# Optimization experiments

Hardware: AMD Instinct MI355X
Metric: run time of the kernel (lower is better)

The kernel has to match this reference:

```python
import jax, jax.numpy as jnp
import numpy as np

B, KL, XL, DIM, H, PB = 4, 128, 4096, 256, 8, 8
HD = DIM // H
SCALE = HD ** -0.5
N_DIS = 64 + 2


def setup_inputs() -> dict:
    key = jax.random.key(0)
    ks = jax.random.split(key, 10)
    x = jax.random.normal(ks[0], (B, XL, DIM), jnp.float32)
    kernal = jax.random.normal(ks[1], (B, KL, DIM), jnp.float32)
    rd = jax.random.randint(ks[2], (B, KL, XL), 0, N_DIS)
    polar_pos = jax.random.randint(ks[3], (B, KL, XL), 0, PB)
    att_mask = jax.random.uniform(ks[4], (B, H, XL, KL)) < 0.1
    W_qkv = jax.random.normal(ks[5], (DIM, 3 * DIM), jnp.float32) * 0.02
    dis_embed = jax.random.normal(ks[6], (N_DIS, H), jnp.float32) * 0.02
    polar_emb = jax.random.normal(ks[7], (PB, 1), jnp.float32) * 0.02
    W_proj = jax.random.normal(ks[8], (DIM, DIM), jnp.float32) * 0.02
    b_proj = jnp.zeros((DIM,), jnp.float32)
    return dict(x=x, kernal=kernal, rd=rd, polar_pos=polar_pos, att_mask=att_mask,
                W_qkv=W_qkv, dis_embed=dis_embed, polar_emb=polar_emb,
                W_proj=W_proj, b_proj=b_proj)


def _heads(t, h):
    b, n, d = t.shape
    return t.reshape(b, n, h, d // h).transpose(0, 2, 1, 3)  # b h n hd


def reference(x, kernal, rd, polar_pos, att_mask, W_qkv, dis_embed, polar_emb, W_proj, b_proj):
    b, xl, dim = x.shape
    kl = kernal.shape[1]
    h = H
    scale = (dim // h) ** -0.5

    q, k, v = [_heads(t, h) for t in jnp.split(x @ W_qkv, 3, axis=-1)]        # b h xl hd
    k_q, k_k, k_v = [_heads(t, h) for t in jnp.split(kernal @ W_qkv, 3, axis=-1)]  # b h kl hd

    rd_e = dis_embed[rd].transpose(0, 3, 1, 2)  # (b,kl,xl,h) -> (b,h,kl,xl)

    # kernel -> x attention scores
    k_x_attn = jnp.einsum('bhkd,bhxd->bhkx', k_q, k) * scale  # b h kl xl

    # main orientation: one-hot-weighted |attn| reduced over x, argmax over polar bins
    pp = jnp.broadcast_to(polar_pos[:, None], (b, h, kl, xl))  # b h kl xl
    polar_hot = jax.nn.one_hot(pp, PB, dtype=k_x_attn.dtype)   # b h kl xl o
    ori_sum = jnp.einsum('bhkx,bhkxo->bhko', jnp.abs(k_x_attn), polar_hot)
    main_ori = jnp.argmax(ori_sum, axis=-1)                    # b h kl
    new_polar = pp - main_ori[..., None]
    new_polar = jnp.where(new_polar < 0, new_polar + PB, new_polar)
    polar_bias = polar_emb[new_polar, 0]                       # b h kl xl

    mask_k = att_mask.transpose(0, 1, 3, 2)                    # b h kl xl
    k_x_attn = jnp.where(mask_k, jnp.asarray(-1e6, k_x_attn.dtype), k_x_attn)
    attn_k = jax.nn.softmax(k_x_attn + rd_e + polar_bias, axis=-1)
    k_out = jnp.einsum('bhkx,bhxd->bhkd', attn_k, v)
    k_out = k_out.transpose(0, 2, 1, 3).reshape(b, kl, dim) @ W_proj + b_proj

    # x -> kernel attention scores
    x_k_attn = jnp.einsum('bhxd,bhkd->bhxk', q, k_k) * scale   # b h xl kl
    x_k_attn = jnp.where(att_mask, jnp.asarray(-1e9, x_k_attn.dtype), x_k_attn)
    x_k_attn = jax.nn.softmax(x_k_attn + rd_e.transpose(0, 1, 3, 2)
                              + polar_bias.transpose(0, 1, 3, 2), axis=-1)
    x_out = jnp.einsum('bhxk,bhkd->bhxd', x_k_attn, k_v)
    x_out = x_out.transpose(0, 2, 1, 3).reshape(b, xl, dim) @ W_proj + b_proj

    return (x_out, k_out)
```

## Files before the change

### kernel.cpp

```cpp
#include <hip/hip_runtime.h>
#include <hip/hip_bf16.h>

#define B_    4
#define KL_   128
#define XL_   4096
#define DIM_  256
#define H_    8
#define HD_   32
#define PB_   8
#define NDIS_ 66
#define TDIM_ 768
#define SCALE_ 0.17677669529663687f
#define NS_   4
#define XCH_  (XL_ / NS_)
#define NCH2_ 64
#define KC2_  16

typedef float v4f __attribute__((ext_vector_type(4)));
typedef short v8s __attribute__((ext_vector_type(8)));

__device__ __forceinline__ unsigned short f2bf(float f) {
    __hip_bfloat16 h = __float2bfloat16(f);
    return __builtin_bit_cast(unsigned short, h);
}
__device__ __forceinline__ float bf2f(unsigned short u) {
    return __bfloat162float(__builtin_bit_cast(__hip_bfloat16, u));
}
__device__ __forceinline__ void cvt_hilo(float v, unsigned short& hi, unsigned short& lo) {
    hi = f2bf(v);
    lo = f2bf(v - bf2f(hi));
}

__global__ __launch_bounds__(256) void pack_mask(const int* __restrict__ att_mask,
                                                 unsigned int* __restrict__ mbits) {
    size_t wid = (size_t)blockIdx.x * 256 + threadIdx.x;
    const int* src = &att_mask[wid * 32];
    unsigned bits = 0;
#pragma unroll
    for (int i = 0; i < 8; ++i) {
        int4 m4 = *(const int4*)&src[i * 4];
        bits |= (m4.x ? 1u : 0u) << (i * 4 + 0);
        bits |= (m4.y ? 1u : 0u) << (i * 4 + 1);
        bits |= (m4.z ? 1u : 0u) << (i * 4 + 2);
        bits |= (m4.w ? 1u : 0u) << (i * 4 + 3);
    }
    mbits[wid] = bits;
}

__global__ __launch_bounds__(256) void cvt_mat(const float* __restrict__ A,
                                               unsigned short* __restrict__ Ah,
                                               unsigned short* __restrict__ Al,
                                               size_t n4) {
    size_t i = ((size_t)blockIdx.x * 256 + threadIdx.x);
    if (i >= n4) return;
    float4 v = *(const float4*)&A[i * 4];
    ushort4 h, l;
    cvt_hilo(v.x, h.x, l.x);
    cvt_hilo(v.y, h.y, l.y);
    cvt_hilo(v.z, h.z, l.z);
    cvt_hilo(v.w, h.w, l.w);
    *(ushort4*)&Ah[i * 4] = h;
    *(ushort4*)&Al[i * 4] = l;
}

__global__ __launch_bounds__(256) void cvt_wT(const float* __restrict__ W,
                                              unsigned short* __restrict__ Wh,
                                              unsigned short* __restrict__ Wl,
                                              int K, int N) {
    int n = blockIdx.x, k = threadIdx.x;
    float v = W[(size_t)k * N + n];
    unsigned short h, l;
    cvt_hilo(v, h, l);
    Wh[(size_t)n * K + k] = h;
    Wl[(size_t)n * K + k] = l;
}

__global__ __launch_bounds__(256) void cvt_kq(const float* __restrict__ qkv_k,
                                              unsigned short* __restrict__ Kqh_g,
                                              unsigned short* __restrict__ Kql_g,
                                              unsigned short* __restrict__ Kk_bf,
                                              unsigned short* __restrict__ VT_bf) {
    const int bh = blockIdx.x;
    const int b = bh >> 3, h = bh & 7;
    const int tid = threadIdx.x;
    const int k = tid >> 1, dg = (tid & 1) * 16;
    const float* src = &qkv_k[((size_t)(b * KL_ + k)) * TDIM_ + h * HD_ + dg];
    unsigned short hi[16], lo[16];
#pragma unroll
    for (int j4 = 0; j4 < 4; ++j4) {
        float4 v = *(const float4*)&src[j4 * 4];
        cvt_hilo(v.x, hi[j4 * 4 + 0], lo[j4 * 4 + 0]);
        cvt_hilo(v.y, hi[j4 * 4 + 1], lo[j4 * 4 + 1]);
        cvt_hilo(v.z, hi[j4 * 4 + 2], lo[j4 * 4 + 2]);
        cvt_hilo(v.w, hi[j4 * 4 + 3], lo[j4 * 4 + 3]);
    }
    unsigned short* dh = &Kqh_g[((size_t)bh * KL_ + k) * HD_ + dg];
    unsigned short* dl = &Kql_g[((size_t)bh * KL_ + k) * HD_ + dg];
    *(uint4*)&dh[0] = *(uint4*)&hi[0];
    *(uint4*)&dh[8] = *(uint4*)&hi[8];
    *(uint4*)&dl[0] = *(uint4*)&lo[0];
    *(uint4*)&dl[8] = *(uint4*)&lo[8];
    unsigned short kk[16];
#pragma unroll
    for (int j4 = 0; j4 < 4; ++j4) {
        float4 v = *(const float4*)&src[DIM_ + j4 * 4];
        kk[j4 * 4 + 0] = f2bf(v.x);
        kk[j4 * 4 + 1] = f2bf(v.y);
        kk[j4 * 4 + 2] = f2bf(v.z);
        kk[j4 * 4 + 3] = f2bf(v.w);
    }
    unsigned short* dk = &Kk_bf[((size_t)bh * KL_ + k) * HD_ + dg];
    *(uint4*)&dk[0] = *(uint4*)&kk[0];
    *(uint4*)&dk[8] = *(uint4*)&kk[8];
#pragma unroll
    for (int j = 0; j < 16; ++j)
        VT_bf[((size_t)bh * HD_ + dg + j) * KL_ + k] = f2bf(src[2 * DIM_ + j]);
}

__global__ __launch_bounds__(256) void gemm_mfma(const unsigned short* __restrict__ Ah,
                                                 const unsigned short* __restrict__ Al,
                                                 const unsigned short* __restrict__ Bh,
                                                 const unsigned short* __restrict__ Bl,
                                                 float* __restrict__ C,
                                                 const float* __restrict__ bias,
                                                 int M, int N, int K) {
    __shared__ __align__(16) unsigned short Ah_s[128 * 32];
    __shared__ __align__(16) unsigned short Al_s[128 * 32];
    __shared__ __align__(16) unsigned short Bh_s[128 * 32];
    __shared__ __align__(16) unsigned short Bl_s[128 * 32];
    const int tid = threadIdx.x;
    const int w = tid >> 6, lane = tid & 63;
    const int c = lane & 15, q = lane >> 4;
    const int bm = blockIdx.y * 128, bn = blockIdx.x * 128;

    const int lrow = lane >> 2;
    const int lcol = (lane & 3) * 8;

    v4f acc[2][8] = {};
    for (int k0 = 0; k0 < K; k0 += 32) {
        __syncthreads();
#pragma unroll
        for (int i = 0; i < 2; ++i) {
            const int chunk = w * 2 + i;
            const int row = chunk * 16 + lrow;
            const size_t ga = (size_t)(bm + row) * K + k0 + lcol;
            const size_t gb = (size_t)(bn + row) * K + k0 + lcol;
            const int lo = chunk * 512;
            __builtin_amdgcn_global_load_lds(
                (const __attribute__((address_space(1))) unsigned int*)&Ah[ga],
                (__attribute__((address_space(3))) unsigned int*)&Ah_s[lo], 16, 0, 0);
            __builtin_amdgcn_global_load_lds(
                (const __attribute__((address_space(1))) unsigned int*)&Al[ga],
                (__attribute__((address_space(3))) unsigned int*)&Al_s[lo], 16, 0, 0);
            __builtin_amdgcn_global_load_lds(
                (const __attribute__((address_space(1))) unsigned int*)&Bh[gb],
                (__attribute__((address_space(3))) unsigned int*)&Bh_s[lo], 16, 0, 0);
            __builtin_amdgcn_global_load_lds(
                (const __attribute__((address_space(1))) unsigned int*)&Bl[gb],
                (__attribute__((address_space(3))) unsigned int*)&Bl_s[lo], 16, 0, 0);
        }
        asm volatile("s_waitcnt vmcnt(0)" ::: "memory");
        __syncthreads();
        v8s afh[2], afl[2];
#pragma unroll
        for (int mt = 0; mt < 2; ++mt) {
            afh[mt] = *(v8s*)&Ah_s[(w * 32 + mt * 16 + c) * 32 + q * 8];
            afl[mt] = *(v8s*)&Al_s[(w * 32 + mt * 16 + c) * 32 + q * 8];
        }
#pragma unroll
        for (int nt = 0; nt < 8; ++nt) {
            v8s bfh = *(v8s*)&Bh_s[(nt * 16 + c) * 32 + q * 8];
            v8s bfl = *(v8s*)&Bl_s[(nt * 16 + c) * 32 + q * 8];
#pragma unroll
            for (int mt = 0; mt < 2; ++mt) {
                acc[mt][nt] = __builtin_amdgcn_mfma_f32_16x16x32_bf16(afl[mt], bfh, acc[mt][nt], 0, 0, 0);
                acc[mt][nt] = __builtin_amdgcn_mfma_f32_16x16x32_bf16(afh[mt], bfl, acc[mt][nt], 0, 0, 0);
                acc[mt][nt] = __builtin_amdgcn_mfma_f32_16x16x32_bf16(afh[mt], bfh, acc[mt][nt], 0, 0, 0);
            }
        }
    }
#pragma unroll
    for (int mt = 0; mt < 2; ++mt) {
#pragma unroll
        for (int nt = 0; nt < 8; ++nt) {
            int col = bn + nt * 16 + c;
            float bv = bias ? bias[col] : 0.0f;
#pragma unroll
            for (int r = 0; r < 4; ++r) {
                int row = bm + w * 32 + mt * 16 + q * 4 + r;
                C[(size_t)row * N + col] = acc[mt][nt][r] + bv;
            }
        }
    }
}

__global__ __launch_bounds__(256) void gemm64(const float* __restrict__ A,
                                              const float* __restrict__ Bw,
                                              float* __restrict__ C,
                                              const float* __restrict__ bias,
                                              int M, int N, int K) {
    __shared__ __align__(16) float As[16][68];
    __shared__ __align__(16) float Bs[16][64];
    const int tid = threadIdx.x;
    const int tx = tid & 15, ty = tid >> 4;
    const int bn = blockIdx.x * 64, bm = blockIdx.y * 64;
    const int am = tid >> 2, ac = tid & 3;
    float acc[4][4] = {};
    for (int k0 = 0; k0 < K; k0 += 16) {
        float4 a4 = *(const float4*)&A[(size_t)(bm + am) * K + k0 + ac * 4];
        As[ac * 4 + 0][am] = a4.x;
        As[ac * 4 + 1][am] = a4.y;
        As[ac * 4 + 2][am] = a4.z;
        As[ac * 4 + 3][am] = a4.w;
        *(float4*)&Bs[ty][tx * 4] = *(const float4*)&Bw[(size_t)(k0 + ty) * N + bn + tx * 4];
        __syncthreads();
#pragma unroll
        for (int kk = 0; kk < 16; ++kk) {
            float4 av = *(const float4*)&As[kk][ty * 4];
            float4 bv = *(const float4*)&Bs[kk][tx * 4];
            float a[4] = {av.x, av.y, av.z, av.w};
            float b[4] = {bv.x, bv.y, bv.z, bv.w};
#pragma unroll
            for (int i = 0; i < 4; ++i)
#pragma unroll
                for (int j = 0; j < 4; ++j) acc[i][j] += a[i] * b[j];
        }
        __syncthreads();
    }
#pragma unroll
    for (int i = 0; i < 4; ++i) {
        int m = bm + ty * 4 + i;
#pragma unroll
        for (int j = 0; j < 4; ++j) {
            int n = bn + tx * 4 + j;
            float v = acc[i][j];
            if (bias) v += bias[n];
            C[(size_t)m * N + n] = v;
        }
    }
}

__global__ __launch_bounds__(256) void score_bins_mfma4(const float* __restrict__ qkv_x,
                                                        const unsigned short* __restrict__ Kqh_g,
                                                        const unsigned short* __restrict__ Kql_g,
                                                        const int* __restrict__ rd,
                                                        const int* __restrict__ polar_pos,
                                                        const unsigned int* __restrict__ mbits,
                                                        const float* __restrict__ dis_embed,
                                                        __hip_bfloat16* __restrict__ Sg,
                                                        float* __restrict__ binspart) {
    const int b = blockIdx.z, h = blockIdx.y, xc = blockIdx.x;
    const int x0 = xc * 64;
    const int tid = threadIdx.x;
    const int w = tid >> 6, lane = tid & 63;
    const int c15 = lane & 15, q = lane >> 4;
    const size_t bh = (size_t)(b * H_ + h);

    __shared__ unsigned int mskb[64][5];
    __shared__ float de_h[NDIS_];
    __shared__ float binsL[8][4][16][PB_];
    __shared__ __align__(16) unsigned short Ss[2][16][72];

    {
        int xr = tid >> 2, kg = tid & 3;
        mskb[xr][kg] = mbits[(bh * XL_ + x0 + xr) * 4 + kg];
    }
    if (tid < NDIS_) de_h[tid] = dis_embed[tid * H_ + h];
    __syncthreads();

    v8s axh, axl;
    {
        const float* src = &qkv_x[((size_t)b * XL_ + x0 + w * 16 + c15) * TDIM_ + DIM_ + h * HD_ + q * 8];
        float4 v0 = *(const float4*)&src[0];
        float4 v1 = *(const float4*)&src[4];
        float vv[8] = {v0.x, v0.y, v0.z, v0.w, v1.x, v1.y, v1.z, v1.w};
#pragma unroll
        for (int j = 0; j < 8; ++j) {
            unsigned short hi, lo;
            cvt_hilo(vv[j], hi, lo);
            ((short*)&axh)[j] = (short)hi;
            ((short*)&axl)[j] = (short)lo;
        }
    }

    v8s bqh[2], bql[2];
    int4 r4[2], p4[2];
    auto load_nt = [&](int nt, int s) {
        const int k = nt * 16 + c15;
        const size_t kqoff = (bh * KL_ + k) * HD_ + q * 8;
        bqh[s] = *(const v8s*)&Kqh_g[kqoff];
        bql[s] = *(const v8s*)&Kql_g[kqoff];
        const size_t rowoff = ((size_t)(b * KL_ + k)) * XL_ + x0 + w * 16 + q * 4;
        r4[s] = *(const int4*)&rd[rowoff];
        p4[s] = *(const int4*)&polar_pos[rowoff];
    };
    load_nt(0, 0);

#pragma unroll
    for (int nt = 0; nt < 8; ++nt) {
        const int s = nt & 1;
        if (nt < 7) load_nt(nt + 1, s ^ 1);

        const int k = nt * 16 + c15;
        v4f D = {0.f, 0.f, 0.f, 0.f};
        D = __builtin_amdgcn_mfma_f32_16x16x32_bf16(axl, bqh[s], D, 0, 0, 0);
        D = __builtin_amdgcn_mfma_f32_16x16x32_bf16(axh, bql[s], D, 0, 0, 0);
        D = __builtin_amdgcn_mfma_f32_16x16x32_bf16(axh, bqh[s], D, 0, 0, 0);

        float bins[PB_] = {};
        {
            int rv[4] = {r4[s].x, r4[s].y, r4[s].z, r4[s].w};
            int pv[4] = {p4[s].x, p4[s].y, p4[s].z, p4[s].w};
            ushort4 pack;
#pragma unroll
            for (int r = 0; r < 4; ++r) {
                float sc = D[r] * SCALE_;
                float a = fabsf(sc);
                int pp = pv[r];
#pragma unroll
                for (int pb = 0; pb < PB_; ++pb) bins[pb] += (pp == pb) ? a : 0.0f;
                int xloc = w * 16 + q * 4 + r;
                int mbit = (mskb[xloc][k >> 5] >> (k & 31)) & 1;
                float sp = (mbit ? -1e6f : sc) + de_h[rv[r]];
                ((unsigned short*)&pack)[r] = f2bf(sp);
            }
            *(ushort4*)&Ss[s][c15][w * 16 + q * 4] = pack;
        }

#pragma unroll
        for (int pb = 0; pb < PB_; ++pb) {
            bins[pb] += __shfl_xor(bins[pb], 16);
            bins[pb] += __shfl_xor(bins[pb], 32);
        }
        if (q == 0) {
#pragma unroll
            for (int pb = 0; pb < PB_; ++pb) binsL[nt][w][c15][pb] = bins[pb];
        }

        __syncthreads();
        {
            int row = tid >> 4, seg = tid & 15;
            unsigned short* dst = (unsigned short*)Sg +
                (bh * KL_ + nt * 16 + row) * XL_ + x0 + seg * 4;
            *(uint2*)dst = *(const uint2*)&Ss[s][row][seg * 4];
        }
    }
    __syncthreads();
    {
        int k = tid >> 1, half = tid & 1;
        int nt = k >> 4, c = k & 15;
        float4 s = {0.f, 0.f, 0.f, 0.f};
#pragma unroll
        for (int w4 = 0; w4 < 4; ++w4) {
            float4 v = *(float4*)&binsL[nt][w4][c][half * 4];
            s.x += v.x; s.y += v.y; s.z += v.z; s.w += v.w;
        }
        *(float4*)&binspart[(bh * KL_ + k) * (NCH2_ * PB_) + xc * PB_ + half * 4] = s;
    }
}

__global__ __launch_bounds__(256) void bins_argmax(const float* __restrict__ binspart,
                                                   int* __restrict__ main_ori) {
    const int w = threadIdx.x >> 6, lane = threadIdx.x & 63;
    const int row = blockIdx.x * 4 + w;
    float s[PB_];
#pragma unroll
    for (int pb = 0; pb < PB_; ++pb) s[pb] = 0.0f;
    if (lane < NCH2_) {
        const float* bp = &binspart[(size_t)row * (NCH2_ * PB_) + lane * PB_];
#pragma unroll
        for (int pb = 0; pb < PB_; ++pb) s[pb] = bp[pb];
    }
#pragma unroll
    for (int m = 1; m < 64; m <<= 1)
#pragma unroll
        for (int pb = 0; pb < PB_; ++pb) s[pb] += __shfl_xor(s[pb], m);
    if (lane == 0) {
        float best = s[0];
        int bi = 0;
#pragma unroll
        for (int pb = 1; pb < PB_; ++pb)
            if (s[pb] > best) { best = s[pb]; bi = pb; }
        main_ori[row] = bi;
    }
}

__global__ __launch_bounds__(256) void flash_cached2(const float* __restrict__ qkv_x,
                                                     const __hip_bfloat16* __restrict__ Sg,
                                                     const int* __restrict__ polar_pos,
                                                     const float* __restrict__ polar_emb,
                                                     const int* __restrict__ main_ori,
                                                     float* __restrict__ part) {
    const int b = blockIdx.z, h = blockIdx.y;
    const int kch = blockIdx.x / NS_, xc = blockIdx.x % NS_;
    const int k0 = kch * KC2_;
    const int tid = threadIdx.x;
    const int ki = tid >> 4, xt = tid & 15;

    __shared__ __align__(16) float4 vs[64][9];
    __shared__ int pol_s[KC2_][68];
    __shared__ float pe[PB_];

    if (tid < PB_) pe[tid] = polar_emb[tid];
    const size_t xbase = (size_t)b * XL_;
    const size_t bh = (size_t)(b * H_ + h);
    const size_t row_k = bh * KL_ + k0 + ki;
    const int mo = main_ori[row_k];
    const int xbeg = xc * XCH_;

    float l = 0.f;
    float4 acc[8] = {};
    __syncthreads();
    for (int t = 0; t < XCH_ / 64; ++t) {
        const int x0 = xbeg + t * 64;
        __syncthreads();
#pragma unroll
        for (int i = 0; i < 2; ++i) {
            int id = tid + 256 * i;
            int row = id >> 3, c = id & 7;
            vs[row][c] = *(const float4*)&qkv_x[(xbase + x0 + row) * TDIM_ + 2 * DIM_ + h * HD_ + c * 4];
        }
        {
            int kk = tid >> 4, c = tid & 15;
            *(int4*)&pol_s[kk][c * 4] =
                *(const int4*)&polar_pos[(size_t)(b * KL_ + k0 + kk) * XL_ + x0 + c * 4];
        }
        __syncthreads();
#pragma unroll
        for (int j = 0; j < 4; ++j) {
            int xl = xt + 16 * j;
            int x = x0 + xl;
            float sp = __bfloat162float(Sg[row_k * XL_ + x]);
            int pp = pol_s[ki][xl];
            int np = pp - mo;
            np += (np >> 31) & PB_;
            float p = __expf(sp + pe[np]);
            l += p;
#pragma unroll
            for (int c = 0; c < 8; ++c) {
                float4 v = vs[xl][c];
                acc[c].x += p * v.x; acc[c].y += p * v.y;
                acc[c].z += p * v.z; acc[c].w += p * v.w;
            }
        }
    }
#pragma unroll
    for (int m = 1; m < 16; m <<= 1) {
        l += __shfl_xor(l, m, 16);
#pragma unroll
        for (int c = 0; c < 8; ++c) {
            acc[c].x += __shfl_xor(acc[c].x, m, 16);
            acc[c].y += __shfl_xor(acc[c].y, m, 16);
            acc[c].z += __shfl_xor(acc[c].z, m, 16);
            acc[c].w += __shfl_xor(acc[c].w, m, 16);
        }
    }
    if (xt == 0) {
        float* dst = &part[(size_t)(row_k * NS_ + xc) * 36];
#pragma unroll
        for (int c = 0; c < 8; ++c) *(float4*)&dst[c * 4] = acc[c];
        dst[32] = l;
    }
}

__global__ __launch_bounds__(256) void merge_cached(const float* __restrict__ part,
                                                    float* __restrict__ kout_pre) {
    const int tid = threadIdx.x;
    const int ri = tid >> 5, d = tid & 31;
    const int row = blockIdx.x * 8 + ri;
    float l = 0.f, a = 0.f;
#pragma unroll
    for (int c = 0; c < NS_; ++c) {
        const float* p = &part[(size_t)(row * NS_ + c) * 36];
        l += p[32];
        a += p[d];
    }
    int k = row & (KL_ - 1);
    int bh = row >> 7;
    int h = bh & (H_ - 1), b = bh >> 3;
    kout_pre[(size_t)(b * KL_ + k) * DIM_ + h * HD_ + d] = a / l;
}

__global__ __launch_bounds__(256) void attn_x_mfma(const float* __restrict__ qkv_x,
                                                   const unsigned short* __restrict__ Kk_bf,
                                                   const unsigned short* __restrict__ VT_bf,
                                                   const int* __restrict__ rd,
                                                   const int* __restrict__ polar_pos,
                                                   const unsigned int* __restrict__ mbits,
                                                   const float* __restrict__ dis_embed,
                                                   const float* __restrict__ polar_emb,
                                                   const int* __restrict__ main_ori,
                                                   unsigned short* __restrict__ oh,
                                                   unsigned short* __restrict__ ol) {
    const int b = blockIdx.z, h = blockIdx.y;
    const int x0 = blockIdx.x * 64;
    const int tid = threadIdx.x;
    const int wave = tid >> 6, lane = tid & 63;
    const int c = lane & 15, q = lane >> 4;

    __shared__ __align__(16) unsigned short P_s[4][16][136];
    __shared__ unsigned short rp_s[KL_][72];
    __shared__ unsigned int msk_s[64][5];
    __shared__ float de_h[NDIS_];
    __shared__ float pe[PB_];
    __shared__ int mo_s[KL_];

    const size_t bh = (size_t)(b * H_ + h);
    if (tid < NDIS_) de_h[tid] = dis_embed[tid * H_ + h];
    if (tid < PB_) pe[tid] = polar_emb[tid];
    if (tid < KL_) mo_s[tid] = main_ori[bh * KL_ + tid];
    {
        int xr = tid >> 2, kg = tid & 3;
        msk_s[xr][kg] = mbits[(bh * XL_ + x0 + xr) * 4 + kg];
    }
    __syncthreads();

#pragma unroll
    for (int i = 0; i < 8; ++i) {
        int id = tid + 256 * i;
        int k = id >> 4, cc = id & 15;
        size_t gb = (size_t)(b * KL_ + k) * XL_ + x0 + cc * 4;
        int4 r4 = *(const int4*)&rd[gb];
        int4 p4 = *(const int4*)&polar_pos[gb];
        int mo = mo_s[k];
        int n0 = p4.x - mo; n0 += (n0 >> 31) & PB_;
        int n1 = p4.y - mo; n1 += (n1 >> 31) & PB_;
        int n2 = p4.z - mo; n2 += (n2 >> 31) & PB_;
        int n3 = p4.w - mo; n3 += (n3 >> 31) & PB_;
        rp_s[k][cc * 4 + 0] = (unsigned short)(r4.x | (n0 << 8));
        rp_s[k][cc * 4 + 1] = (unsigned short)(r4.y | (n1 << 8));
        rp_s[k][cc * 4 + 2] = (unsigned short)(r4.z | (n2 << 8));
        rp_s[k][cc * 4 + 3] = (unsigned short)(r4.w | (n3 << 8));
    }
    __syncthreads();

    v8s aq;
    {
        const float* qp = &qkv_x[(size_t)(b * XL_ + x0 + wave * 16 + c) * TDIM_ + h * HD_ + q * 8];
        float4 q0 = *(const float4*)&qp[0];
        float4 q1 = *(const float4*)&qp[4];
        aq[0] = (short)f2bf(q0.x); aq[1] = (short)f2bf(q0.y);
        aq[2] = (short)f2bf(q0.z); aq[3] = (short)f2bf(q0.w);
        aq[4] = (short)f2bf(q1.x); aq[5] = (short)f2bf(q1.y);
        aq[6] = (short)f2bf(q1.z); aq[7] = (short)f2bf(q1.w);
    }

    const unsigned short* KkB = &Kk_bf[(size_t)bh * KL_ * HD_];
    v4f S[8];
#pragma unroll
    for (int t = 0; t < 8; ++t) {
        v8s bk = *(const v8s*)&KkB[(size_t)(t * 16 + c) * HD_ + q * 8];
        S[t] = __builtin_amdgcn_mfma_f32_16x16x32_bf16(aq, bk, (v4f){0.f, 0.f, 0.f, 0.f}, 0, 0, 0);
    }

    const int xloc = wave * 16;
    float lr[4] = {0.f, 0.f, 0.f, 0.f};
#pragma unroll
    for (int t = 0; t < 8; ++t) {
#pragma unroll
        for (int r = 0; r < 4; ++r) {
            int krow = t * 16 + c;
            int xrow = q * 4 + r;
            unsigned short rp = rp_s[krow][xloc + xrow];
            int mbit = (msk_s[xloc + xrow][krow >> 5] >> (krow & 31)) & 1;
            float sval = S[t][r] * SCALE_;
            float tval = (mbit ? -25.0f : sval) + de_h[rp & 0x7f] + pe[(rp >> 8) & 7];
            float p = __expf(tval);
            unsigned short pb = f2bf(p);
            P_s[wave][xrow][krow] = pb;
            lr[r] += bf2f(pb);
        }
    }
#pragma unroll
    for (int r = 0; r < 4; ++r) {
#pragma unroll
        for (int m = 1; m < 16; m <<= 1) lr[r] += __shfl_xor(lr[r], m);
    }
    __syncthreads();

    const unsigned short* VTB = &VT_bf[(size_t)bh * HD_ * KL_];
    v4f O0 = {0.f, 0.f, 0.f, 0.f}, O1 = {0.f, 0.f, 0.f, 0.f};
#pragma unroll
    for (int kc = 0; kc < 4; ++kc) {
        v8s ap = *(v8s*)&P_s[wave][c][kc * 32 + q * 8];
        v8s bv0 = *(const v8s*)&VTB[(size_t)c * KL_ + kc * 32 + q * 8];
        v8s bv1 = *(const v8s*)&VTB[(size_t)(16 + c) * KL_ + kc * 32 + q * 8];
        O0 = __builtin_amdgcn_mfma_f32_16x16x32_bf16(ap, bv0, O0, 0, 0, 0);
        O1 = __builtin_amdgcn_mfma_f32_16x16x32_bf16(ap, bv1, O1, 0, 0, 0);
    }

#pragma unroll
    for (int r = 0; r < 4; ++r) {
        int xg = x0 + wave * 16 + q * 4 + r;
        float inv = 1.0f / lr[r];
        size_t obase = (size_t)(b * XL_ + xg) * DIM_ + h * HD_;
        float v0 = O0[r] * inv;
        float v1 = O1[r] * inv;
        unsigned short h0, l0, h1, l1;
        cvt_hilo(v0, h0, l0);
        cvt_hilo(v1, h1, l1);
        oh[obase + c] = h0;
        ol[obase + c] = l0;
        oh[obase + 16 + c] = h1;
        ol[obase + 16 + c] = l1;
    }
}

extern "C" void kernel_launch(void* const* d_in, const int* in_sizes, int n_in,
                              void* d_out, int out_size, void* d_ws, size_t ws_size,
                              hipStream_t stream) {
    const float* x         = (const float*)d_in[0];
    const float* kernal    = (const float*)d_in[1];
    const int* rd          = (const int*)d_in[2];
    const int* polar_pos   = (const int*)d_in[3];
    const int* att_mask    = (const int*)d_in[4];
    const float* W_qkv     = (const float*)d_in[5];
    const float* dis_embed = (const float*)d_in[6];
    const float* polar_emb = (const float*)d_in[7];
    const float* W_proj    = (const float*)d_in[8];
    const float* b_proj    = (const float*)d_in[9];
    float* out             = (float*)d_out;

    char* base = (char*)d_ws;
    size_t off = 0;
    auto alloc = [&](size_t bytes) { void* p = base + off; off = (off + bytes + 255) & ~255ULL; return p; };
    float* qkv_x    = (float*)alloc((size_t)B_ * XL_ * TDIM_ * 4);
    float* qkv_k    = (float*)alloc((size_t)B_ * KL_ * TDIM_ * 4);
    float* xout_pre = (float*)alloc((size_t)B_ * XL_ * DIM_ * 4);
    float* kout_pre = (float*)alloc((size_t)B_ * KL_ * DIM_ * 4);
    int* main_ori   = (int*)alloc(B_ * H_ * KL_ * 4);
    float* part     = (float*)alloc((size_t)B_ * H_ * KL_ * NS_ * 36 * 4);
    __hip_bfloat16* Sg = (__hip_bfloat16*)alloc((size_t)B_ * H_ * KL_ * XL_ * 2);
    unsigned short* wph = (unsigned short*)alloc((size_t)DIM_ * DIM_ * 2);
    unsigned short* wpl = (unsigned short*)alloc((size_t)DIM_ * DIM_ * 2);
    unsigned int* mbits = (unsigned int*)alloc((size_t)B_ * H_ * XL_ * (KL_ / 32) * 4);
    unsigned short* Kk_bf = (unsigned short*)alloc((size_t)B_ * H_ * KL_ * HD_ * 2);
    unsigned short* VT_bf = (unsigned short*)alloc((size_t)B_ * H_ * HD_ * KL_ * 2);

    float* binspart = xout_pre;
    const size_t MX = (size_t)B_ * XL_;
    unsigned short* xh = (unsigned short*)Sg;
    unsigned short* xl_ = xh + MX * DIM_;
    unsigned short* wqh = (unsigned short*)part;
    unsigned short* wql = wqh + (size_t)TDIM_ * DIM_;
    unsigned short* kqh_g = wqh + 2 * (size_t)TDIM_ * DIM_;
    unsigned short* kql_g = kqh_g + (size_t)B_ * H_ * KL_ * HD_;
    unsigned short* oh = (unsigned short*)Sg;
    unsigned short* ol = oh + MX * DIM_;

    pack_mask<<<dim3((B_ * H_ * XL_ * (KL_ / 32)) / 256), 256, 0, stream>>>(att_mask, mbits);
    cvt_mat<<<dim3((MX * DIM_ / 4 + 255) / 256), 256, 0, stream>>>(x, xh, xl_, MX * DIM_ / 4);
    cvt_wT<<<dim3(TDIM_), DIM_, 0, stream>>>(W_qkv, wqh, wql, DIM_, TDIM_);
    cvt_wT<<<dim3(DIM_), DIM_, 0, stream>>>(W_proj, wph, wpl, DIM_, DIM_);

    gemm_mfma<<<dim3(TDIM_ / 128, MX / 128), 256, 0, stream>>>(
        xh, xl_, wqh, wql, qkv_x, nullptr, MX, TDIM_, DIM_);
    gemm64<<<dim3(TDIM_ / 64, (B_ * KL_) / 64), 256, 0, stream>>>(
        kernal, W_qkv, qkv_k, nullptr, B_ * KL_, TDIM_, DIM_);
    cvt_kq<<<dim3(B_ * H_), 256, 0, stream>>>(qkv_k, kqh_g, kql_g, Kk_bf, VT_bf);

    score_bins_mfma4<<<dim3(NCH2_, H_, B_), 256, 0, stream>>>(
        qkv_x, kqh_g, kql_g, rd, polar_pos, mbits, dis_embed, Sg, binspart);
    bins_argmax<<<dim3(B_ * H_ * KL_ / 4), 256, 0, stream>>>(binspart, main_ori);
    flash_cached2<<<dim3((KL_ / KC2_) * NS_, H_, B_), 256, 0, stream>>>(
        qkv_x, Sg, polar_pos, polar_emb, main_ori, part);
    merge_cached<<<dim3(B_ * H_ * KL_ / 8), 256, 0, stream>>>(part, kout_pre);

    attn_x_mfma<<<dim3(XL_ / 64, H_, B_), 256, 0, stream>>>(
        qkv_x, Kk_bf, VT_bf, rd, polar_pos, mbits, dis_embed, polar_emb, main_ori, oh, ol);

    gemm_mfma<<<dim3(DIM_ / 128, MX / 128), 256, 0, stream>>>(
        oh, ol, wph, wpl, out, b_proj, MX, DIM_, DIM_);
    gemm64<<<dim3(DIM_ / 64, (B_ * KL_) / 64), 256, 0, stream>>>(
        kout_pre, W_proj, out + (size_t)B_ * XL_ * DIM_, b_proj, B_ * KL_, DIM_, DIM_);
}
```

Baseline: 345.9 us.

## Fuse preprocessing kernels and emit bf16 Q/K splits directly from QKV GEMM epilogues

```diff
diff --git a/kernel.cpp b/kernel.cpp
--- a/kernel.cpp
+++ b/kernel.cpp
@@ -16,6 +16,11 @@
 #define NCH2_ 64
 #define KC2_  16
 
+#define NB_CVT_  4096
+#define NB_PACK_ 2048
+#define NB_WQ_   768
+#define NB_WP_   256
+
 typedef float v4f __attribute__((ext_vector_type(4)));
 typedef short v8s __attribute__((ext_vector_type(8)));
 
@@ -31,90 +36,56 @@
     lo = f2bf(v - bf2f(hi));
 }
 
-__global__ __launch_bounds__(256) void pack_mask(const int* __restrict__ att_mask,
-                                                 unsigned int* __restrict__ mbits) {
-    size_t wid = (size_t)blockIdx.x * 256 + threadIdx.x;
-    const int* src = &att_mask[wid * 32];
-    unsigned bits = 0;
-#pragma unroll
-    for (int i = 0; i < 8; ++i) {
-        int4 m4 = *(const int4*)&src[i * 4];
-        bits |= (m4.x ? 1u : 0u) << (i * 4 + 0);
-        bits |= (m4.y ? 1u : 0u) << (i * 4 + 1);
-        bits |= (m4.z ? 1u : 0u) << (i * 4 + 2);
-        bits |= (m4.w ? 1u : 0u) << (i * 4 + 3);
-    }
-    mbits[wid] = bits;
-}
-
-__global__ __launch_bounds__(256) void cvt_mat(const float* __restrict__ A,
-                                               unsigned short* __restrict__ Ah,
-                                               unsigned short* __restrict__ Al,
-                                               size_t n4) {
-    size_t i = ((size_t)blockIdx.x * 256 + threadIdx.x);
-    if (i >= n4) return;
-    float4 v = *(const float4*)&A[i * 4];
-    ushort4 h, l;
-    cvt_hilo(v.x, h.x, l.x);
-    cvt_hilo(v.y, h.y, l.y);
-    cvt_hilo(v.z, h.z, l.z);
-    cvt_hilo(v.w, h.w, l.w);
-    *(ushort4*)&Ah[i * 4] = h;
-    *(ushort4*)&Al[i * 4] = l;
-}
-
-__global__ __launch_bounds__(256) void cvt_wT(const float* __restrict__ W,
-                                              unsigned short* __restrict__ Wh,
-                                              unsigned short* __restrict__ Wl,
-                                              int K, int N) {
-    int n = blockIdx.x, k = threadIdx.x;
-    float v = W[(size_t)k * N + n];
-    unsigned short h, l;
-    cvt_hilo(v, h, l);
-    Wh[(size_t)n * K + k] = h;
-    Wl[(size_t)n * K + k] = l;
-}
-
-__global__ __launch_bounds__(256) void cvt_kq(const float* __restrict__ qkv_k,
-                                              unsigned short* __restrict__ Kqh_g,
-                                              unsigned short* __restrict__ Kql_g,
-                                              unsigned short* __restrict__ Kk_bf,
-                                              unsigned short* __restrict__ VT_bf) {
-    const int bh = blockIdx.x;
-    const int b = bh >> 3, h = bh & 7;
-    const int tid = threadIdx.x;
-    const int k = tid >> 1, dg = (tid & 1) * 16;
-    const float* src = &qkv_k[((size_t)(b * KL_ + k)) * TDIM_ + h * HD_ + dg];
-    unsigned short hi[16], lo[16];
-#pragma unroll
-    for (int j4 = 0; j4 < 4; ++j4) {
-        float4 v = *(const float4*)&src[j4 * 4];
-        cvt_hilo(v.x, hi[j4 * 4 + 0], lo[j4 * 4 + 0]);
-        cvt_hilo(v.y, hi[j4 * 4 + 1], lo[j4 * 4 + 1]);
-        cvt_hilo(v.z, hi[j4 * 4 + 2], lo[j4 * 4 + 2]);
-        cvt_hilo(v.w, hi[j4 * 4 + 3], lo[j4 * 4 + 3]);
-    }
-    unsigned short* dh = &Kqh_g[((size_t)bh * KL_ + k) * HD_ + dg];
-    unsigned short* dl = &Kql_g[((size_t)bh * KL_ + k) * HD_ + dg];
-    *(uint4*)&dh[0] = *(uint4*)&hi[0];
-    *(uint4*)&dh[8] = *(uint4*)&hi[8];
-    *(uint4*)&dl[0] = *(uint4*)&lo[0];
-    *(uint4*)&dl[8] = *(uint4*)&lo[8];
-    unsigned short kk[16];
-#pragma unroll
-    for (int j4 = 0; j4 < 4; ++j4) {
-        float4 v = *(const float4*)&src[DIM_ + j4 * 4];
-        kk[j4 * 4 + 0] = f2bf(v.x);
-        kk[j4 * 4 + 1] = f2bf(v.y);
-        kk[j4 * 4 + 2] = f2bf(v.z);
-        kk[j4 * 4 + 3] = f2bf(v.w);
-    }
-    unsigned short* dk = &Kk_bf[((size_t)bh * KL_ + k) * HD_ + dg];
-    *(uint4*)&dk[0] = *(uint4*)&kk[0];
-    *(uint4*)&dk[8] = *(uint4*)&kk[8];
-#pragma unroll
-    for (int j = 0; j < 16; ++j)
-        VT_bf[((size_t)bh * HD_ + dg + j) * KL_ + k] = f2bf(src[2 * DIM_ + j]);
+__global__ __launch_bounds__(256) void preamble(const float* __restrict__ x,
+                                                const int* __restrict__ att_mask,
+                                                const float* __restrict__ W_qkv,
+                                                const float* __restrict__ W_proj,
+                                                unsigned short* __restrict__ xh,
+                                                unsigned short* __restrict__ xl,
+                                                unsigned int* __restrict__ mbits,
+                                                unsigned short* __restrict__ wqh,
+                                                unsigned short* __restrict__ wql,
+                                                unsigned short* __restrict__ wph,
+                                                unsigned short* __restrict__ wpl) {
+    const int bid = blockIdx.x, tid = threadIdx.x;
+    if (bid < NB_CVT_) {
+        size_t i = (size_t)bid * 256 + tid;
+        float4 v = *(const float4*)&x[i * 4];
+        ushort4 h, l;
+        cvt_hilo(v.x, h.x, l.x);
+        cvt_hilo(v.y, h.y, l.y);
+        cvt_hilo(v.z, h.z, l.z);
+        cvt_hilo(v.w, h.w, l.w);
+        *(ushort4*)&xh[i * 4] = h;
+        *(ushort4*)&xl[i * 4] = l;
+    } else if (bid < NB_CVT_ + NB_PACK_) {
+        size_t wid = (size_t)(bid - NB_CVT_) * 256 + tid;
+        const int* src = &att_mask[wid * 32];
+        unsigned bits = 0;
+#pragma unroll
+        for (int i = 0; i < 8; ++i) {
+            int4 m4 = *(const int4*)&src[i * 4];
+            bits |= (m4.x ? 1u : 0u) << (i * 4 + 0);
+            bits |= (m4.y ? 1u : 0u) << (i * 4 + 1);
+            bits |= (m4.z ? 1u : 0u) << (i * 4 + 2);
+            bits |= (m4.w ? 1u : 0u) << (i * 4 + 3);
+        }
+        mbits[wid] = bits;
+    } else if (bid < NB_CVT_ + NB_PACK_ + NB_WQ_) {
+        int n = bid - (NB_CVT_ + NB_PACK_), k = tid;
+        float v = W_qkv[(size_t)k * TDIM_ + n];
+        unsigned short h, l;
+        cvt_hilo(v, h, l);
+        wqh[(size_t)n * DIM_ + k] = h;
+        wql[(size_t)n * DIM_ + k] = l;
+    } else {
+        int n = bid - (NB_CVT_ + NB_PACK_ + NB_WQ_), k = tid;
+        float v = W_proj[(size_t)k * DIM_ + n];
+        unsigned short h, l;
+        cvt_hilo(v, h, l);
+        wph[(size_t)n * DIM_ + k] = h;
+        wpl[(size_t)n * DIM_ + k] = l;
+    }
 }
 
 __global__ __launch_bounds__(256) void gemm_mfma(const unsigned short* __restrict__ Ah,
@@ -123,7 +94,11 @@
                                                  const unsigned short* __restrict__ Bl,
                                                  float* __restrict__ C,
                                                  const float* __restrict__ bias,
-                                                 int M, int N, int K) {
+                                                 int M, int N, int K, int mode,
+                                                 unsigned short* __restrict__ qh,
+                                                 unsigned short* __restrict__ kh,
+                                                 unsigned short* __restrict__ kl2,
+                                                 float* __restrict__ vx) {
     __shared__ __align__(16) unsigned short Ah_s[128 * 32];
     __shared__ __align__(16) unsigned short Al_s[128 * 32];
     __shared__ __align__(16) unsigned short Bh_s[128 * 32];
@@ -179,16 +154,41 @@
             }
         }
     }
-#pragma unroll
-    for (int mt = 0; mt < 2; ++mt) {
-#pragma unroll
-        for (int nt = 0; nt < 8; ++nt) {
-            int col = bn + nt * 16 + c;
-            float bv = bias ? bias[col] : 0.0f;
-#pragma unroll
-            for (int r = 0; r < 4; ++r) {
-                int row = bm + w * 32 + mt * 16 + q * 4 + r;
-                C[(size_t)row * N + col] = acc[mt][nt][r] + bv;
+    if (mode == 0) {
+#pragma unroll
+        for (int mt = 0; mt < 2; ++mt) {
+#pragma unroll
+            for (int nt = 0; nt < 8; ++nt) {
+                int col = bn + nt * 16 + c;
+                float bv = bias ? bias[col] : 0.0f;
+#pragma unroll
+                for (int r = 0; r < 4; ++r) {
+                    int row = bm + w * 32 + mt * 16 + q * 4 + r;
+                    C[(size_t)row * N + col] = acc[mt][nt][r] + bv;
+                }
+            }
+        }
+    } else {
+#pragma unroll
+        for (int mt = 0; mt < 2; ++mt) {
+#pragma unroll
+            for (int nt = 0; nt < 8; ++nt) {
+                int col = bn + nt * 16 + c;
+#pragma unroll
+                for (int r = 0; r < 4; ++r) {
+                    int row = bm + w * 32 + mt * 16 + q * 4 + r;
+                    float v = acc[mt][nt][r];
+                    if (col < DIM_) {
+                        qh[(size_t)row * DIM_ + col] = f2bf(v);
+                    } else if (col < 2 * DIM_) {
+                        unsigned short hi, lo;
+                        cvt_hilo(v, hi, lo);
+                        kh[(size_t)row * DIM_ + col - DIM_] = hi;
+                        kl2[(size_t)row * DIM_ + col - DIM_] = lo;
+                    } else {
+                        vx[(size_t)row * DIM_ + col - 2 * DIM_] = v;
+                    }
+                }
             }
         }
     }
@@ -240,7 +240,69 @@
     }
 }
 
-__global__ __launch_bounds__(256) void score_bins_mfma4(const float* __restrict__ qkv_x,
+__global__ __launch_bounds__(256) void gemm64_qkv(const float* __restrict__ A,
+                                                  const float* __restrict__ Bw,
+                                                  unsigned short* __restrict__ Kqh,
+                                                  unsigned short* __restrict__ Kql,
+                                                  unsigned short* __restrict__ Kk_bf,
+                                                  unsigned short* __restrict__ VT_bf,
+                                                  int M, int N, int K) {
+    __shared__ __align__(16) float As[16][68];
+    __shared__ __align__(16) float Bs[16][64];
+    const int tid = threadIdx.x;
+    const int tx = tid & 15, ty = tid >> 4;
+    const int bn = blockIdx.x * 64, bm = blockIdx.y * 64;
+    const int am = tid >> 2, ac = tid & 3;
+    float acc[4][4] = {};
+    for (int k0 = 0; k0 < K; k0 += 16) {
+        float4 a4 = *(const float4*)&A[(size_t)(bm + am) * K + k0 + ac * 4];
+        As[ac * 4 + 0][am] = a4.x;
+        As[ac * 4 + 1][am] = a4.y;
+        As[ac * 4 + 2][am] = a4.z;
+        As[ac * 4 + 3][am] = a4.w;
+        *(float4*)&Bs[ty][tx * 4] = *(const float4*)&Bw[(size_t)(k0 + ty) * N + bn + tx * 4];
+        __syncthreads();
+#pragma unroll
+        for (int kk = 0; kk < 16; ++kk) {
+            float4 av = *(const float4*)&As[kk][ty * 4];
+            float4 bv = *(const float4*)&Bs[kk][tx * 4];
+            float a[4] = {av.x, av.y, av.z, av.w};
+            float b[4] = {bv.x, bv.y, bv.z, bv.w};
+#pragma unroll
+            for (int i = 0; i < 4; ++i)
+#pragma unroll
+                for (int j = 0; j < 4; ++j) acc[i][j] += a[i] * b[j];
+        }
+        __syncthreads();
+    }
+#pragma unroll
+    for (int i = 0; i < 4; ++i) {
+        int m = bm + ty * 4 + i;
+        int b = m >> 7, k = m & 127;
+#pragma unroll
+        for (int j = 0; j < 4; ++j) {
+            int n = bn + tx * 4 + j;
+            float v = acc[i][j];
+            if (n < DIM_) {
+                unsigned short hi, lo;
+                cvt_hilo(v, hi, lo);
+                int h = n >> 5, d = n & 31;
+                size_t o = ((size_t)(b * H_ + h) * KL_ + k) * HD_ + d;
+                Kqh[o] = hi;
+                Kql[o] = lo;
+            } else if (n < 2 * DIM_) {
+                int nn = n - DIM_, h = nn >> 5, d = nn & 31;
+                Kk_bf[((size_t)(b * H_ + h) * KL_ + k) * HD_ + d] = f2bf(v);
+            } else {
+                int nn = n - 2 * DIM_, h = nn >> 5, d = nn & 31;
+                VT_bf[((size_t)(b * H_ + h) * HD_ + d) * KL_ + k] = f2bf(v);
+            }
+        }
+    }
+}
+
+__global__ __launch_bounds__(256) void score_bins_mfma4(const unsigned short* __restrict__ kxh,
+                                                        const unsigned short* __restrict__ kxl,
                                                         const unsigned short* __restrict__ Kqh_g,
                                                         const unsigned short* __restrict__ Kql_g,
                                                         const int* __restrict__ rd,
@@ -258,7 +320,7 @@
 
     __shared__ unsigned int mskb[64][5];
     __shared__ float de_h[NDIS_];
-    __shared__ float binsL[8][4][16][PB_];
+    __shared__ float binsL[8][4][16][PB_ + 1];
     __shared__ __align__(16) unsigned short Ss[2][16][72];
 
     {
@@ -270,17 +332,9 @@
 
     v8s axh, axl;
     {
-        const float* src = &qkv_x[((size_t)b * XL_ + x0 + w * 16 + c15) * TDIM_ + DIM_ + h * HD_ + q * 8];
-        float4 v0 = *(const float4*)&src[0];
-        float4 v1 = *(const float4*)&src[4];
-        float vv[8] = {v0.x, v0.y, v0.z, v0.w, v1.x, v1.y, v1.z, v1.w};
-#pragma unroll
-        for (int j = 0; j < 8; ++j) {
-            unsigned short hi, lo;
-            cvt_hilo(vv[j], hi, lo);
-            ((short*)&axh)[j] = (short)hi;
-            ((short*)&axl)[j] = (short)lo;
-        }
+        const size_t aoff = ((size_t)b * XL_ + x0 + w * 16 + c15) * DIM_ + h * HD_ + q * 8;
+        axh = *(const v8s*)&kxh[aoff];
+        axl = *(const v8s*)&kxl[aoff];
     }
 
     v8s bqh[2], bql[2];
@@ -352,8 +406,8 @@
         float4 s = {0.f, 0.f, 0.f, 0.f};
 #pragma unroll
         for (int w4 = 0; w4 < 4; ++w4) {
-            float4 v = *(float4*)&binsL[nt][w4][c][half * 4];
-            s.x += v.x; s.y += v.y; s.z += v.z; s.w += v.w;
+            const float* bp = &binsL[nt][w4][c][half * 4];
+            s.x += bp[0]; s.y += bp[1]; s.z += bp[2]; s.w += bp[3];
         }
         *(float4*)&binspart[(bh * KL_ + k) * (NCH2_ * PB_) + xc * PB_ + half * 4] = s;
     }
@@ -385,7 +439,7 @@
     }
 }
 
-__global__ __launch_bounds__(256) void flash_cached2(const float* __restrict__ qkv_x,
+__global__ __launch_bounds__(256) void flash_cached2(const float* __restrict__ vx,
                                                      const __hip_bfloat16* __restrict__ Sg,
                                                      const int* __restrict__ polar_pos,
                                                      const float* __restrict__ polar_emb,
@@ -402,7 +456,6 @@
     __shared__ float pe[PB_];
 
     if (tid < PB_) pe[tid] = polar_emb[tid];
-    const size_t xbase = (size_t)b * XL_;
     const size_t bh = (size_t)(b * H_ + h);
     const size_t row_k = bh * KL_ + k0 + ki;
     const int mo = main_ori[row_k];
@@ -418,7 +471,7 @@
         for (int i = 0; i < 2; ++i) {
             int id = tid + 256 * i;
             int row = id >> 3, c = id & 7;
-            vs[row][c] = *(const float4*)&qkv_x[(xbase + x0 + row) * TDIM_ + 2 * DIM_ + h * HD_ + c * 4];
+            vs[row][c] = *(const float4*)&vx[(size_t)(b * XL_ + x0 + row) * DIM_ + h * HD_ + c * 4];
         }
         {
             int kk = tid >> 4, c = tid & 15;
@@ -481,7 +534,7 @@
     kout_pre[(size_t)(b * KL_ + k) * DIM_ + h * HD_ + d] = a / l;
 }
 
-__global__ __launch_bounds__(256) void attn_x_mfma(const float* __restrict__ qkv_x,
+__global__ __launch_bounds__(256) void attn_x_mfma(const unsigned short* __restrict__ qxh,
                                                    const unsigned short* __restrict__ Kk_bf,
                                                    const unsigned short* __restrict__ VT_bf,
                                                    const int* __restrict__ rd,
@@ -534,16 +587,7 @@
     }
     __syncthreads();
 
-    v8s aq;
-    {
-        const float* qp = &qkv_x[(size_t)(b * XL_ + x0 + wave * 16 + c) * TDIM_ + h * HD_ + q * 8];
-        float4 q0 = *(const float4*)&qp[0];
-        float4 q1 = *(const float4*)&qp[4];
-        aq[0] = (short)f2bf(q0.x); aq[1] = (short)f2bf(q0.y);
-        aq[2] = (short)f2bf(q0.z); aq[3] = (short)f2bf(q0.w);
-        aq[4] = (short)f2bf(q1.x); aq[5] = (short)f2bf(q1.y);
-        aq[6] = (short)f2bf(q1.z); aq[7] = (short)f2bf(q1.w);
-    }
+    v8s aq = *(const v8s*)&qxh[(size_t)(b * XL_ + x0 + wave * 16 + c) * DIM_ + h * HD_ + q * 8];
 
     const unsigned short* KkB = &Kk_bf[(size_t)bh * KL_ * HD_];
     v4f S[8];
@@ -624,53 +668,52 @@
     char* base = (char*)d_ws;
     size_t off = 0;
     auto alloc = [&](size_t bytes) { void* p = base + off; off = (off + bytes + 255) & ~255ULL; return p; };
-    float* qkv_x    = (float*)alloc((size_t)B_ * XL_ * TDIM_ * 4);
-    float* qkv_k    = (float*)alloc((size_t)B_ * KL_ * TDIM_ * 4);
-    float* xout_pre = (float*)alloc((size_t)B_ * XL_ * DIM_ * 4);
-    float* kout_pre = (float*)alloc((size_t)B_ * KL_ * DIM_ * 4);
-    int* main_ori   = (int*)alloc(B_ * H_ * KL_ * 4);
-    float* part     = (float*)alloc((size_t)B_ * H_ * KL_ * NS_ * 36 * 4);
+    const size_t MX = (size_t)B_ * XL_;
+
+    float* vx        = (float*)alloc(MX * DIM_ * 4);
+    unsigned short* qxh = (unsigned short*)alloc(MX * DIM_ * 2);
+    unsigned short* kxh = (unsigned short*)alloc(MX * DIM_ * 2);
+    unsigned short* kxl = (unsigned short*)alloc(MX * DIM_ * 2);
+    float* binspart  = (float*)alloc((size_t)B_ * H_ * KL_ * NCH2_ * PB_ * 4);
+    float* kout_pre  = (float*)alloc((size_t)B_ * KL_ * DIM_ * 4);
+    int* main_ori    = (int*)alloc(B_ * H_ * KL_ * 4);
+    float* part      = (float*)alloc((size_t)B_ * H_ * KL_ * NS_ * 36 * 4);
     __hip_bfloat16* Sg = (__hip_bfloat16*)alloc((size_t)B_ * H_ * KL_ * XL_ * 2);
     unsigned short* wph = (unsigned short*)alloc((size_t)DIM_ * DIM_ * 2);
     unsigned short* wpl = (unsigned short*)alloc((size_t)DIM_ * DIM_ * 2);
+    unsigned short* wqh = (unsigned short*)alloc((size_t)TDIM_ * DIM_ * 2);
+    unsigned short* wql = (unsigned short*)alloc((size_t)TDIM_ * DIM_ * 2);
     unsigned int* mbits = (unsigned int*)alloc((size_t)B_ * H_ * XL_ * (KL_ / 32) * 4);
+    unsigned short* Kqh_g = (unsigned short*)alloc((size_t)B_ * H_ * KL_ * HD_ * 2);
+    unsigned short* Kql_g = (unsigned short*)alloc((size_t)B_ * H_ * KL_ * HD_ * 2);
     unsigned short* Kk_bf = (unsigned short*)alloc((size_t)B_ * H_ * KL_ * HD_ * 2);
     unsigned short* VT_bf = (unsigned short*)alloc((size_t)B_ * H_ * HD_ * KL_ * 2);
 
-    float* binspart = xout_pre;
-    const size_t MX = (size_t)B_ * XL_;
     unsigned short* xh = (unsigned short*)Sg;
     unsigned short* xl_ = xh + MX * DIM_;
-    unsigned short* wqh = (unsigned short*)part;
-    unsigned short* wql = wqh + (size_t)TDIM_ * DIM_;
-    unsigned short* kqh_g = wqh + 2 * (size_t)TDIM_ * DIM_;
-    unsigned short* kql_g = kqh_g + (size_t)B_ * H_ * KL_ * HD_;
     unsigned short* oh = (unsigned short*)Sg;
     unsigned short* ol = oh + MX * DIM_;
 
-    pack_mask<<<dim3((B_ * H_ * XL_ * (KL_ / 32)) / 256), 256, 0, stream>>>(att_mask, mbits);
-    cvt_mat<<<dim3((MX * DIM_ / 4 + 255) / 256), 256, 0, stream>>>(x, xh, xl_, MX * DIM_ / 4);
-    cvt_wT<<<dim3(TDIM_), DIM_, 0, stream>>>(W_qkv, wqh, wql, DIM_, TDIM_);
-    cvt_wT<<<dim3(DIM_), DIM_, 0, stream>>>(W_proj, wph, wpl, DIM_, DIM_);
+    preamble<<<dim3(NB_CVT_ + NB_PACK_ + NB_WQ_ + NB_WP_), 256, 0, stream>>>(
+        x, att_mask, W_qkv, W_proj, xh, xl_, mbits, wqh, wql, wph, wpl);
 
     gemm_mfma<<<dim3(TDIM_ / 128, MX / 128), 256, 0, stream>>>(
-        xh, xl_, wqh, wql, qkv_x, nullptr, MX, TDIM_, DIM_);
-    gemm64<<<dim3(TDIM_ / 64, (B_ * KL_) / 64), 256, 0, stream>>>(
-        kernal, W_qkv, qkv_k, nullptr, B_ * KL_, TDIM_, DIM_);
-    cvt_kq<<<dim3(B_ * H_), 256, 0, stream>>>(qkv_k, kqh_g, kql_g, Kk_bf, VT_bf);
+        xh, xl_, wqh, wql, nullptr, nullptr, MX, TDIM_, DIM_, 1, qxh, kxh, kxl, vx);
+    gemm64_qkv<<<dim3(TDIM_ / 64, (B_ * KL_) / 64), 256, 0, stream>>>(
+        kernal, W_qkv, Kqh_g, Kql_g, Kk_bf, VT_bf, B_ * KL_, TDIM_, DIM_);
 
     score_bins_mfma4<<<dim3(NCH2_, H_, B_), 256, 0, stream>>>(
-        qkv_x, kqh_g, kql_g, rd, polar_pos, mbits, dis_embed, Sg, binspart);
+        kxh, kxl, Kqh_g, Kql_g, rd, polar_pos, mbits, dis_embed, Sg, binspart);
     bins_argmax<<<dim3(B_ * H_ * KL_ / 4), 256, 0, stream>>>(binspart, main_ori);
     flash_cached2<<<dim3((KL_ / KC2_) * NS_, H_, B_), 256, 0, stream>>>(
-        qkv_x, Sg, polar_pos, polar_emb, main_ori, part);
+        vx, Sg, polar_pos, polar_emb, main_ori, part);
     merge_cached<<<dim3(B_ * H_ * KL_ / 8), 256, 0, stream>>>(part, kout_pre);
 
     attn_x_mfma<<<dim3(XL_ / 64, H_, B_), 256, 0, stream>>>(
-        qkv_x, Kk_bf, VT_bf, rd, polar_pos, mbits, dis_embed, polar_emb, main_ori, oh, ol);
+        qxh, Kk_bf, VT_bf, rd, polar_pos, mbits, dis_embed, polar_emb, main_ori, oh, ol);
 
     gemm_mfma<<<dim3(DIM_ / 128, MX / 128), 256, 0, stream>>>(
-        oh, ol, wph, wpl, out, b_proj, MX, DIM_, DIM_);
+        oh, ol, wph, wpl, out, b_proj, MX, DIM_, DIM_, 0, nullptr, nullptr, nullptr, nullptr);
     gemm64<<<dim3(DIM_ / 64, (B_ * KL_) / 64), 256, 0, stream>>>(
         kout_pre, W_proj, out + (size_t)B_ * XL_ * DIM_, b_proj, B_ * KL_, DIM_, DIM_);
 }
```

Result: faster. 335.7 us (-2.9%).
